# Performance work log

Measured on AMD Instinct MI355X. Metric: run time of the kernel, lower is better.

Reference implementation:

```python
import jax, jax.numpy as jnp
import numpy as np

N = 100000          # nodes
E = 600000          # directed edges in real graph
D = 128             # feature dim
LAYER_NUM = 16
ALPHA = 0.15        # args.alpha
DECLINE = 0.9       # args.decline
DECLINE_NEG = 0.5   # args.decline_neg


def setup_inputs() -> dict:
    key = jax.random.key(0)
    k1, k2, k3 = jax.random.split(key, 3)
    feat = jax.random.normal(k1, (N, D), dtype=jnp.float32)
    edge_index = jax.random.randint(k2, (2, E), 0, N, dtype=jnp.int64)
    # 60 sampled negative edges per layer; mirrored in reference -> 120 = round_even(20*E/N)
    neg_edge_index = jax.random.randint(k3, (LAYER_NUM, 2, 60), 0, N, dtype=jnp.int64)
    return {"feat": feat, "edge_index": edge_index, "neg_edge_index": neg_edge_index}


def _spmm(row, col, vals, x, n):
    # y[i] = sum_{e: row[e]==i} vals[e] * x[col[e]]
    return jax.ops.segment_sum(vals[:, None] * x[col], row, num_segments=n)


def reference(feat, edge_index, neg_edge_index):
    n = feat.shape[0]
    row, col = edge_index[0], edge_index[1]
    # symmetric_normalize_adjacency: D^{-1/2} A D^{-1/2} (row-sum degree)
    deg = jax.ops.segment_sum(jnp.ones_like(row, dtype=feat.dtype), row, num_segments=n)
    dis = jnp.where(deg > 0, deg ** -0.5, 0.0)  # guard isolated nodes
    vals = dis[row] * dis[col]

    edge_num = 2 * neg_edge_index.shape[2]  # mirrored -> even, matches (k+1)//2*2
    c = edge_num / n + 2.0                   # re-normalization of (2I - A_neg)

    beta = 1.0
    beta_neg = 1.0
    x = feat
    acc = jnp.zeros_like(feat)
    for l in range(LAYER_NUM):
        # negative adjacency: random edges, symmetrized
        nr = jnp.concatenate([neg_edge_index[l, 0], neg_edge_index[l, 1]])
        nc = jnp.concatenate([neg_edge_index[l, 1], neg_edge_index[l, 0]])
        neg_sp = jax.ops.segment_sum(x[nc], nr, num_segments=n)  # A_neg @ x
        # neg_A_hat = (2I - A_neg)/c ; inv_lazy_A = (1-bn) I + bn neg_A_hat
        inv_x = (1.0 - beta_neg) * x + beta_neg * (2.0 * x - neg_sp) / c
        # lazy_A = (1-b) I + b A_hat
        x = (1.0 - beta) * x + beta * _spmm(row, col, vals, x, n)
        acc = acc + 0.5 * (x + inv_x)
        beta *= DECLINE
        beta_neg *= DECLINE_NEG
    return ALPHA * feat + (1.0 - ALPHA) * (acc / float(LAYER_NUM))
```

## Files before the change

kernel.cpp:

```cpp
#include <hip/hip_runtime.h>
#include <hip/hip_fp16.h>

#define NN 100000
#define NE 600000
#define DD 128
#define NL 16
#define SCAN_B 1024
#define SCAN_NB ((NN + SCAN_B - 1) / SCAN_B)


__global__ void k_deg(const int* __restrict__ ei, int* __restrict__ deg) {
    int e = blockIdx.x * blockDim.x + threadIdx.x;
    if (e < NE) atomicAdd(&deg[ei[e]], 1);
}

__global__ void k_dis(const int* __restrict__ deg, float* __restrict__ dis) {
    int i = blockIdx.x * blockDim.x + threadIdx.x;
    if (i >= NN) return;
    int d = deg[i];
    dis[i] = d > 0 ? rsqrtf((float)d) : 0.f;
}

__global__ void k_bsum(const int* __restrict__ cnt, int* __restrict__ bsum) {
    __shared__ int sh[SCAN_B];
    int i = blockIdx.x * SCAN_B + threadIdx.x;
    sh[threadIdx.x] = (i < NN) ? cnt[i] : 0;
    __syncthreads();
    for (int off = SCAN_B / 2; off > 0; off >>= 1) {
        if (threadIdx.x < off) sh[threadIdx.x] += sh[threadIdx.x + off];
        __syncthreads();
    }
    if (threadIdx.x == 0) bsum[blockIdx.x] = sh[0];
}

__global__ void k_bscan(int* __restrict__ bsum) {
    if (threadIdx.x == 0) {
        int run = 0;
        for (int i = 0; i < SCAN_NB; ++i) { int v = bsum[i]; bsum[i] = run; run += v; }
    }
}

__global__ void k_scan2(const int* __restrict__ cnt, const int* __restrict__ bsum,
                        int* __restrict__ rowptr) {
    __shared__ int sh[SCAN_B];
    int i = blockIdx.x * SCAN_B + threadIdx.x;
    sh[threadIdx.x] = (i < NN) ? cnt[i] : 0;
    __syncthreads();
    for (int off = 1; off < SCAN_B; off <<= 1) {
        int t = (threadIdx.x >= off) ? sh[threadIdx.x - off] : 0;
        __syncthreads();
        sh[threadIdx.x] += t;
        __syncthreads();
    }
    if (i < NN) rowptr[i + 1] = bsum[blockIdx.x] + sh[threadIdx.x];
    if (blockIdx.x == 0 && threadIdx.x == 0) rowptr[0] = 0;
}

__global__ void k_fill(const int* __restrict__ ei, const float* __restrict__ dis,
                       const int* __restrict__ rowptr, int* __restrict__ cursor,
                       int2* __restrict__ edges) {
    int e = blockIdx.x * blockDim.x + threadIdx.x;
    if (e >= NE) return;
    int r = ei[e], c = ei[NE + e];
    float v = dis[r] * dis[c];
    int pos = rowptr[r] + atomicAdd(&cursor[r], 1);
    edges[pos] = make_int2(c, __float_as_int(v));
}

__global__ void k_cvt(const float* __restrict__ f, __half* __restrict__ h) {
    int i = blockIdx.x * blockDim.x + threadIdx.x;
    const float4 v = reinterpret_cast<const float4*>(f)[i];
    __half2 a = __floats2half2_rn(v.x, v.y);
    __half2 b = __floats2half2_rn(v.z, v.w);
    uint2 o;
    o.x = *reinterpret_cast<uint*>(&a);
    o.y = *reinterpret_cast<uint*>(&b);
    reinterpret_cast<uint2*>(h)[i] = o;
}

__device__ __forceinline__ void acc8(float* s, uint4 g, float v) {
    const __half2* h = reinterpret_cast<const __half2*>(&g);
    float2 f0 = __half22float2(h[0]);
    float2 f1 = __half22float2(h[1]);
    float2 f2 = __half22float2(h[2]);
    float2 f3 = __half22float2(h[3]);
    s[0] += v * f0.x; s[1] += v * f0.y; s[2] += v * f1.x; s[3] += v * f1.y;
    s[4] += v * f2.x; s[5] += v * f2.y; s[6] += v * f3.x; s[7] += v * f3.y;
}

template<int MODE>
__global__ __launch_bounds__(256) void k_layer(const int* __restrict__ rowptr,
                                               const int2* __restrict__ edges,
                                               const __half* __restrict__ xo,
                                               __half* __restrict__ xn,
                                               float* __restrict__ acc,
                                               const float* __restrict__ feat,
                                               float fb, float c0, float c1) {
    const int qw = threadIdx.x >> 4;
    const int lane = threadIdx.x & 15;
    const int r = blockIdx.x * 16 + qw;
    if (r >= NN) return;
    int p = rowptr[r];
    const int end = rowptr[r + 1];
    const int d8 = lane * 8;
    float s[8] = {0.f, 0.f, 0.f, 0.f, 0.f, 0.f, 0.f, 0.f};
    for (; p + 3 < end; p += 4) {
        int2 e0 = edges[p];
        int2 e1 = edges[p + 1];
        int2 e2 = edges[p + 2];
        int2 e3 = edges[p + 3];
        const uint4 g0 = *reinterpret_cast<const uint4*>(xo + (size_t)e0.x * DD + d8);
        const uint4 g1 = *reinterpret_cast<const uint4*>(xo + (size_t)e1.x * DD + d8);
        const uint4 g2 = *reinterpret_cast<const uint4*>(xo + (size_t)e2.x * DD + d8);
        const uint4 g3 = *reinterpret_cast<const uint4*>(xo + (size_t)e3.x * DD + d8);
        acc8(s, g0, __int_as_float(e0.y));
        acc8(s, g1, __int_as_float(e1.y));
        acc8(s, g2, __int_as_float(e2.y));
        acc8(s, g3, __int_as_float(e3.y));
    }
    for (; p < end; ++p) {
        int2 ev = edges[p];
        const uint4 gv = *reinterpret_cast<const uint4*>(xo + (size_t)ev.x * DD + d8);
        acc8(s, gv, __int_as_float(ev.y));
    }
    const size_t ih = (size_t)r * DD + d8;
    const uint4 ou = *reinterpret_cast<const uint4*>(xo + ih);
    float o[8];
    {
        const __half2* h = reinterpret_cast<const __half2*>(&ou);
        float2 f0 = __half22float2(h[0]);
        float2 f1 = __half22float2(h[1]);
        float2 f2 = __half22float2(h[2]);
        float2 f3 = __half22float2(h[3]);
        o[0] = f0.x; o[1] = f0.y; o[2] = f1.x; o[3] = f1.y;
        o[4] = f2.x; o[5] = f2.y; o[6] = f3.x; o[7] = f3.y;
    }
    float n[8];
#pragma unroll
    for (int k = 0; k < 8; ++k) n[k] = (1.f - fb) * o[k] + fb * s[k];

    if (MODE == 3) {
        const float4 fA = *reinterpret_cast<const float4*>(feat + ih);
        const float4 fB = *reinterpret_cast<const float4*>(feat + ih + 4);
        const float4 aA = *reinterpret_cast<const float4*>(acc + ih);
        const float4 aB = *reinterpret_cast<const float4*>(acc + ih + 4);
        float4 oA, oB;
        oA.x = 0.15f * fA.x + c0 * (aA.x + 0.5f * n[0]);
        oA.y = 0.15f * fA.y + c0 * (aA.y + 0.5f * n[1]);
        oA.z = 0.15f * fA.z + c0 * (aA.z + 0.5f * n[2]);
        oA.w = 0.15f * fA.w + c0 * (aA.w + 0.5f * n[3]);
        oB.x = 0.15f * fB.x + c0 * (aB.x + 0.5f * n[4]);
        oB.y = 0.15f * fB.y + c0 * (aB.y + 0.5f * n[5]);
        oB.z = 0.15f * fB.z + c0 * (aB.z + 0.5f * n[6]);
        oB.w = 0.15f * fB.w + c0 * (aB.w + 0.5f * n[7]);
        *reinterpret_cast<float4*>(acc + ih) = oA;
        *reinterpret_cast<float4*>(acc + ih + 4) = oB;
    } else {
        __half2 p0 = __floats2half2_rn(n[0], n[1]);
        __half2 p1 = __floats2half2_rn(n[2], n[3]);
        __half2 p2 = __floats2half2_rn(n[4], n[5]);
        __half2 p3 = __floats2half2_rn(n[6], n[7]);
        uint4 w;
        w.x = *reinterpret_cast<uint*>(&p0);
        w.y = *reinterpret_cast<uint*>(&p1);
        w.z = *reinterpret_cast<uint*>(&p2);
        w.w = *reinterpret_cast<uint*>(&p3);
        *reinterpret_cast<uint4*>(xn + ih) = w;
        if (MODE == 1) {
            float4 aA, aB;
            aA.x = c0 * o[0] + c1 * n[0];
            aA.y = c0 * o[1] + c1 * n[1];
            aA.z = c0 * o[2] + c1 * n[2];
            aA.w = c0 * o[3] + c1 * n[3];
            aB.x = c0 * o[4] + c1 * n[4];
            aB.y = c0 * o[5] + c1 * n[5];
            aB.z = c0 * o[6] + c1 * n[6];
            aB.w = c0 * o[7] + c1 * n[7];
            *reinterpret_cast<float4*>(acc + ih) = aA;
            *reinterpret_cast<float4*>(acc + ih + 4) = aB;
        } else if (MODE == 2) {
            float4 aA = *reinterpret_cast<const float4*>(acc + ih);
            float4 aB = *reinterpret_cast<const float4*>(acc + ih + 4);
            aA.x += c0 * o[0] + c1 * n[0];
            aA.y += c0 * o[1] + c1 * n[1];
            aA.z += c0 * o[2] + c1 * n[2];
            aA.w += c0 * o[3] + c1 * n[3];
            aB.x += c0 * o[4] + c1 * n[4];
            aB.y += c0 * o[5] + c1 * n[5];
            aB.z += c0 * o[6] + c1 * n[6];
            aB.w += c0 * o[7] + c1 * n[7];
            *reinterpret_cast<float4*>(acc + ih) = aA;
            *reinterpret_cast<float4*>(acc + ih + 4) = aB;
        }
    }
}

__global__ void k_neg(const int* __restrict__ nl, const __half* __restrict__ x,
                      float* __restrict__ acc, float coef) {
    int tid = blockIdx.x * blockDim.x + threadIdx.x;
    int e = tid >> 5;
    if (e >= 120) return;
    int d4 = (tid & 31) << 2;
    int r = nl[e];
    int c = (e < 60) ? nl[60 + e] : nl[e - 60];
    const uint2 g = *reinterpret_cast<const uint2*>(x + (size_t)c * DD + d4);
    const __half2* h = reinterpret_cast<const __half2*>(&g);
    float2 f0 = __half22float2(h[0]);
    float2 f1 = __half22float2(h[1]);
    float* ap = acc + (size_t)r * DD + d4;
    atomicAdd(ap + 0, coef * f0.x);
    atomicAdd(ap + 1, coef * f0.y);
    atomicAdd(ap + 2, coef * f1.x);
    atomicAdd(ap + 3, coef * f1.y);
}

extern "C" void kernel_launch(void* const* d_in, const int* in_sizes, int n_in,
                              void* d_out, int out_size, void* d_ws, size_t ws_size,
                              hipStream_t stream) {
    const float* feat = (const float*)d_in[0];
    const int* ei = (const int*)d_in[1];
    const int* negei = (const int*)d_in[2];
    float* out = (float*)d_out;

    __half* xh0 = (__half*)d_ws;
    __half* xha = xh0 + (size_t)NN * DD;
    __half* xhb = xha + (size_t)NN * DD;
    int2* edges = (int2*)(xhb + (size_t)NN * DD);
    int* rowptr = (int*)(edges + NE);
    int* deg = rowptr + (NN + 1);
    float* dis = (float*)(deg + NN);
    int* bsum = (int*)(dis + NN);

    hipMemsetAsync(deg, 0, NN * sizeof(int), stream);
    k_deg<<<(NE + 255) / 256, 256, 0, stream>>>(ei, deg);
    k_dis<<<(NN + 255) / 256, 256, 0, stream>>>(deg, dis);
    k_bsum<<<SCAN_NB, SCAN_B, 0, stream>>>(deg, bsum);
    k_bscan<<<1, 64, 0, stream>>>(bsum);
    k_scan2<<<SCAN_NB, SCAN_B, 0, stream>>>(deg, bsum, rowptr);
    hipMemsetAsync(deg, 0, NN * sizeof(int), stream);
    k_fill<<<(NE + 255) / 256, 256, 0, stream>>>(ei, dis, rowptr, deg, edges);
    k_cvt<<<(NN * DD / 4) / 256, 256, 0, stream>>>(feat, xh0);

    const double cc = 120.0 / 100000.0 + 2.0;
    double bv[NL], coef[NL + 1], negco[NL];
    {
        double b = 1.0, bn = 1.0;
        for (int l = 0; l < NL; ++l) {
            double al = (1.0 - bn) + 2.0 * bn / cc;
            bv[l] = b;
            coef[l] = 0.5 * al + (l > 0 ? 0.5 : 0.0);
            negco[l] = -0.5 * bn / cc;
            b *= 0.9;
            bn *= 0.5;
        }
    }

    const int lg = (NN + 15) / 16;

    for (int l = 0; l < NL - 1; ++l) {
        const __half* xo = (l == 0) ? xh0 : ((l & 1) ? xha : xhb);
        __half* xn = (l & 1) ? xhb : xha;
        float fb = (float)bv[l];
        if (l == 0) {
            k_layer<1><<<lg, 256, 0, stream>>>(rowptr, edges, xo, xn, out, feat,
                                               fb, (float)coef[0], (float)coef[1]);
        } else if ((l & 1) == 0) {
            k_layer<2><<<lg, 256, 0, stream>>>(rowptr, edges, xo, xn, out, feat,
                                               fb, (float)coef[l], (float)coef[l + 1]);
        } else {
            k_layer<0><<<lg, 256, 0, stream>>>(rowptr, edges, xo, xn, out, feat,
                                               fb, 0.f, 0.f);
        }
        k_neg<<<(120 * 32 + 255) / 256, 256, 0, stream>>>(negei + l * 120, xo, out,
                                                          (float)negco[l]);
    }
    {
        const __half* xo = xha;
        k_neg<<<(120 * 32 + 255) / 256, 256, 0, stream>>>(negei + 15 * 120, xo, out,
                                                          (float)negco[15]);
        k_layer<3><<<lg, 256, 0, stream>>>(rowptr, edges, xo, nullptr, out, feat,
                                           (float)bv[15], 0.85f / 16.f, 0.f);
    }
}
```

Baseline: 725.9 us.

## Split feature dimension into 32-wide chunks so each layer's working set fits cache

Runs the whole 16-layer propagation separately for each of four 32-column feature slices. Each slice uses compact half-precision ping-pong buffers and a float accumulator, which should shrink the gathered working set enough to stay L2/MALL resident. Within a row, four groups of lanes now split the edge list and combine partial sums with shuffles. The cost is four times as many kernel launches, and each slice re-reads the CSR edges and row pointers.

```diff
diff --git a/kernel.cpp b/kernel.cpp
--- a/kernel.cpp
+++ b/kernel.cpp
@@ -5,6 +5,8 @@
 #define NE 600000
 #define DD 128
 #define NL 16
+#define CW 32
+#define NCH (DD / CW)
 #define SCAN_B 1024
 #define SCAN_NB ((NN + SCAN_B - 1) / SCAN_B)
 
@@ -67,15 +69,23 @@
     edges[pos] = make_int2(c, __float_as_int(v));
 }
 
-__global__ void k_cvt(const float* __restrict__ f, __half* __restrict__ h) {
-    int i = blockIdx.x * blockDim.x + threadIdx.x;
-    const float4 v = reinterpret_cast<const float4*>(f)[i];
-    __half2 a = __floats2half2_rn(v.x, v.y);
-    __half2 b = __floats2half2_rn(v.z, v.w);
-    uint2 o;
-    o.x = *reinterpret_cast<uint*>(&a);
-    o.y = *reinterpret_cast<uint*>(&b);
-    reinterpret_cast<uint2*>(h)[i] = o;
+__global__ void k_cvt_slice(const float* __restrict__ feat, __half* __restrict__ xc,
+                            int chunk) {
+    int t = blockIdx.x * blockDim.x + threadIdx.x;
+    if (t >= NN * 4) return;
+    int row = t >> 2, q = t & 3;
+    const float4 a = *reinterpret_cast<const float4*>(feat + (size_t)row * DD + chunk * CW + q * 8);
+    const float4 b = *reinterpret_cast<const float4*>(feat + (size_t)row * DD + chunk * CW + q * 8 + 4);
+    __half2 h0 = __floats2half2_rn(a.x, a.y);
+    __half2 h1 = __floats2half2_rn(a.z, a.w);
+    __half2 h2 = __floats2half2_rn(b.x, b.y);
+    __half2 h3 = __floats2half2_rn(b.z, b.w);
+    uint4 w;
+    w.x = *reinterpret_cast<uint*>(&h0);
+    w.y = *reinterpret_cast<uint*>(&h1);
+    w.z = *reinterpret_cast<uint*>(&h2);
+    w.w = *reinterpret_cast<uint*>(&h3);
+    *reinterpret_cast<uint4*>(xc + (size_t)row * CW + q * 8) = w;
 }
 
 __device__ __forceinline__ void acc8(float* s, uint4 g, float v) {
@@ -95,35 +105,38 @@
                                                __half* __restrict__ xn,
                                                float* __restrict__ acc,
                                                const float* __restrict__ feat,
-                                               float fb, float c0, float c1) {
-    const int qw = threadIdx.x >> 4;
-    const int lane = threadIdx.x & 15;
-    const int r = blockIdx.x * 16 + qw;
-    if (r >= NN) return;
-    int p = rowptr[r];
+                                               float* __restrict__ out,
+                                               float fb, float c0, float c1,
+                                               int chunk) {
+    const int tid = threadIdx.x;
+    const int r = blockIdx.x * 16 + (tid >> 4);
+    const int g = (tid >> 2) & 3;
+    const int q = tid & 3;
+    const int beg = rowptr[r];
     const int end = rowptr[r + 1];
-    const int d8 = lane * 8;
     float s[8] = {0.f, 0.f, 0.f, 0.f, 0.f, 0.f, 0.f, 0.f};
-    for (; p + 3 < end; p += 4) {
+    int p = beg + g;
+    for (; p + 4 < end; p += 8) {
         int2 e0 = edges[p];
-        int2 e1 = edges[p + 1];
-        int2 e2 = edges[p + 2];
-        int2 e3 = edges[p + 3];
-        const uint4 g0 = *reinterpret_cast<const uint4*>(xo + (size_t)e0.x * DD + d8);
-        const uint4 g1 = *reinterpret_cast<const uint4*>(xo + (size_t)e1.x * DD + d8);
-        const uint4 g2 = *reinterpret_cast<const uint4*>(xo + (size_t)e2.x * DD + d8);
-        const uint4 g3 = *reinterpret_cast<const uint4*>(xo + (size_t)e3.x * DD + d8);
+        int2 e1 = edges[p + 4];
+        const uint4 g0 = *reinterpret_cast<const uint4*>(xo + (size_t)e0.x * CW + q * 8);
+        const uint4 g1 = *reinterpret_cast<const uint4*>(xo + (size_t)e1.x * CW + q * 8);
         acc8(s, g0, __int_as_float(e0.y));
         acc8(s, g1, __int_as_float(e1.y));
-        acc8(s, g2, __int_as_float(e2.y));
-        acc8(s, g3, __int_as_float(e3.y));
-    }
-    for (; p < end; ++p) {
+    }
+    if (p < end) {
         int2 ev = edges[p];
-        const uint4 gv = *reinterpret_cast<const uint4*>(xo + (size_t)ev.x * DD + d8);
+        const uint4 gv = *reinterpret_cast<const uint4*>(xo + (size_t)ev.x * CW + q * 8);
         acc8(s, gv, __int_as_float(ev.y));
     }
-    const size_t ih = (size_t)r * DD + d8;
+#pragma unroll
+    for (int k = 0; k < 8; ++k) {
+        s[k] += __shfl_xor(s[k], 4);
+        s[k] += __shfl_xor(s[k], 8);
+    }
+    if (g != 0) return;
+
+    const size_t ih = (size_t)r * CW + q * 8;
     const uint4 ou = *reinterpret_cast<const uint4*>(xo + ih);
     float o[8];
     {
@@ -140,8 +153,9 @@
     for (int k = 0; k < 8; ++k) n[k] = (1.f - fb) * o[k] + fb * s[k];
 
     if (MODE == 3) {
-        const float4 fA = *reinterpret_cast<const float4*>(feat + ih);
-        const float4 fB = *reinterpret_cast<const float4*>(feat + ih + 4);
+        const size_t fi = (size_t)r * DD + chunk * CW + q * 8;
+        const float4 fA = *reinterpret_cast<const float4*>(feat + fi);
+        const float4 fB = *reinterpret_cast<const float4*>(feat + fi + 4);
         const float4 aA = *reinterpret_cast<const float4*>(acc + ih);
         const float4 aB = *reinterpret_cast<const float4*>(acc + ih + 4);
         float4 oA, oB;
@@ -153,8 +167,8 @@
         oB.y = 0.15f * fB.y + c0 * (aB.y + 0.5f * n[5]);
         oB.z = 0.15f * fB.z + c0 * (aB.z + 0.5f * n[6]);
         oB.w = 0.15f * fB.w + c0 * (aB.w + 0.5f * n[7]);
-        *reinterpret_cast<float4*>(acc + ih) = oA;
-        *reinterpret_cast<float4*>(acc + ih + 4) = oB;
+        *reinterpret_cast<float4*>(out + fi) = oA;
+        *reinterpret_cast<float4*>(out + fi + 4) = oB;
     } else {
         __half2 p0 = __floats2half2_rn(n[0], n[1]);
         __half2 p1 = __floats2half2_rn(n[2], n[3]);
@@ -198,16 +212,16 @@
 __global__ void k_neg(const int* __restrict__ nl, const __half* __restrict__ x,
                       float* __restrict__ acc, float coef) {
     int tid = blockIdx.x * blockDim.x + threadIdx.x;
-    int e = tid >> 5;
-    if (e >= 120) return;
-    int d4 = (tid & 31) << 2;
+    if (tid >= 120 * 8) return;
+    int e = tid >> 3;
+    int t8 = tid & 7;
     int r = nl[e];
     int c = (e < 60) ? nl[60 + e] : nl[e - 60];
-    const uint2 g = *reinterpret_cast<const uint2*>(x + (size_t)c * DD + d4);
+    const uint2 g = *reinterpret_cast<const uint2*>(x + (size_t)c * CW + t8 * 4);
     const __half2* h = reinterpret_cast<const __half2*>(&g);
     float2 f0 = __half22float2(h[0]);
     float2 f1 = __half22float2(h[1]);
-    float* ap = acc + (size_t)r * DD + d4;
+    float* ap = acc + (size_t)r * CW + t8 * 4;
     atomicAdd(ap + 0, coef * f0.x);
     atomicAdd(ap + 1, coef * f0.y);
     atomicAdd(ap + 2, coef * f1.x);
@@ -222,10 +236,11 @@
     const int* negei = (const int*)d_in[2];
     float* out = (float*)d_out;
 
-    __half* xh0 = (__half*)d_ws;
-    __half* xha = xh0 + (size_t)NN * DD;
-    __half* xhb = xha + (size_t)NN * DD;
-    int2* edges = (int2*)(xhb + (size_t)NN * DD);
+    __half* xc0 = (__half*)d_ws;
+    __half* xca = xc0 + (size_t)NN * CW;
+    __half* xcb = xca + (size_t)NN * CW;
+    float* accc = (float*)(xcb + (size_t)NN * CW);
+    int2* edges = (int2*)(accc + (size_t)NN * CW);
     int* rowptr = (int*)(edges + NE);
     int* deg = rowptr + (NN + 1);
     float* dis = (float*)(deg + NN);
@@ -239,7 +254,6 @@
     k_scan2<<<SCAN_NB, SCAN_B, 0, stream>>>(deg, bsum, rowptr);
     hipMemsetAsync(deg, 0, NN * sizeof(int), stream);
     k_fill<<<(NE + 255) / 256, 256, 0, stream>>>(ei, dis, rowptr, deg, edges);
-    k_cvt<<<(NN * DD / 4) / 256, 256, 0, stream>>>(feat, xh0);
 
     const double cc = 120.0 / 100000.0 + 2.0;
     double bv[NL], coef[NL + 1], negco[NL];
@@ -255,30 +269,33 @@
         }
     }
 
-    const int lg = (NN + 15) / 16;
-
-    for (int l = 0; l < NL - 1; ++l) {
-        const __half* xo = (l == 0) ? xh0 : ((l & 1) ? xha : xhb);
-        __half* xn = (l & 1) ? xhb : xha;
-        float fb = (float)bv[l];
-        if (l == 0) {
-            k_layer<1><<<lg, 256, 0, stream>>>(rowptr, edges, xo, xn, out, feat,
-                                               fb, (float)coef[0], (float)coef[1]);
-        } else if ((l & 1) == 0) {
-            k_layer<2><<<lg, 256, 0, stream>>>(rowptr, edges, xo, xn, out, feat,
-                                               fb, (float)coef[l], (float)coef[l + 1]);
-        } else {
-            k_layer<0><<<lg, 256, 0, stream>>>(rowptr, edges, xo, xn, out, feat,
-                                               fb, 0.f, 0.f);
+    const int lg = NN / 16;
+    const int cg = (NN * 4 + 255) / 256;
+    const int ng = (120 * 8 + 255) / 256;
+
+    for (int ch = 0; ch < NCH; ++ch) {
+        k_cvt_slice<<<cg, 256, 0, stream>>>(feat, xc0, ch);
+        for (int l = 0; l < NL - 1; ++l) {
+            const __half* xo = (l == 0) ? xc0 : ((l & 1) ? xca : xcb);
+            __half* xn = (l & 1) ? xcb : xca;
+            float fb = (float)bv[l];
+            if (l == 0) {
+                k_layer<1><<<lg, 256, 0, stream>>>(rowptr, edges, xo, xn, accc, feat, out,
+                                                   fb, (float)coef[0], (float)coef[1], ch);
+            } else if ((l & 1) == 0) {
+                k_layer<2><<<lg, 256, 0, stream>>>(rowptr, edges, xo, xn, accc, feat, out,
+                                                   fb, (float)coef[l], (float)coef[l + 1], ch);
+            } else {
+                k_layer<0><<<lg, 256, 0, stream>>>(rowptr, edges, xo, xn, accc, feat, out,
+                                                   fb, 0.f, 0.f, ch);
+            }
+            k_neg<<<ng, 256, 0, stream>>>(negei + l * 120, xo, accc, (float)negco[l]);
         }
-        k_neg<<<(120 * 32 + 255) / 256, 256, 0, stream>>>(negei + l * 120, xo, out,
-                                                          (float)negco[l]);
-    }
-    {
-        const __half* xo = xha;
-        k_neg<<<(120 * 32 + 255) / 256, 256, 0, stream>>>(negei + 15 * 120, xo, out,
-                                                          (float)negco[15]);
-        k_layer<3><<<lg, 256, 0, stream>>>(rowptr, edges, xo, nullptr, out, feat,
-                                           (float)bv[15], 0.85f / 16.f, 0.f);
-    }
-}
+        {
+            const __half* xo = xca;
+            k_neg<<<ng, 256, 0, stream>>>(negei + 15 * 120, xo, accc, (float)negco[15]);
+            k_layer<3><<<lg, 256, 0, stream>>>(rowptr, edges, xo, nullptr, accc, feat, out,
+                                               (float)bv[15], 0.85f / 16.f, 0.f, ch);
+        }
+    }
+}
```

New measurement: 1.247 ms. +71.8%, slower.

## Batch accumulator updates every four layers using a four-buffer feature ring

Applied to the files above, without the earlier changes.

Keeps four fp16 feature buffers in a ring so the fp32 accumulator is read and written once every four layers instead of every other layer. Each accumulating layer reads the two earlier snapshots and folds their contributions in. The 60-edge negative-sample scatter kernels are merged into one launch per four layers, and the separate dis kernel and the second memset are removed by computing rsqrt inside the fill kernel. The cost is extra fp16 reads of xm2 and xm1 in the accumulating layers, one more N×D fp16 buffer of workspace, and dropping the row bounds check, which relies on N being divisible by 16.

```diff
diff --git a/kernel.cpp b/kernel.cpp
--- a/kernel.cpp
+++ b/kernel.cpp
@@ -12,13 +12,6 @@
 __global__ void k_deg(const int* __restrict__ ei, int* __restrict__ deg) {
     int e = blockIdx.x * blockDim.x + threadIdx.x;
     if (e < NE) atomicAdd(&deg[ei[e]], 1);
-}
-
-__global__ void k_dis(const int* __restrict__ deg, float* __restrict__ dis) {
-    int i = blockIdx.x * blockDim.x + threadIdx.x;
-    if (i >= NN) return;
-    int d = deg[i];
-    dis[i] = d > 0 ? rsqrtf((float)d) : 0.f;
 }
 
 __global__ void k_bsum(const int* __restrict__ cnt, int* __restrict__ bsum) {
@@ -56,13 +49,14 @@
     if (blockIdx.x == 0 && threadIdx.x == 0) rowptr[0] = 0;
 }
 
-__global__ void k_fill(const int* __restrict__ ei, const float* __restrict__ dis,
+__global__ void k_fill(const int* __restrict__ ei, const int* __restrict__ deg,
                        const int* __restrict__ rowptr, int* __restrict__ cursor,
                        int2* __restrict__ edges) {
     int e = blockIdx.x * blockDim.x + threadIdx.x;
     if (e >= NE) return;
     int r = ei[e], c = ei[NE + e];
-    float v = dis[r] * dis[c];
+    int dr = deg[r], dc = deg[c];
+    float v = (dr > 0 ? rsqrtf((float)dr) : 0.f) * (dc > 0 ? rsqrtf((float)dc) : 0.f);
     int pos = rowptr[r] + atomicAdd(&cursor[r], 1);
     edges[pos] = make_int2(c, __float_as_int(v));
 }
@@ -88,18 +82,30 @@
     s[4] += v * f2.x; s[5] += v * f2.y; s[6] += v * f3.x; s[7] += v * f3.y;
 }
 
+__device__ __forceinline__ void cvt8(float* o, uint4 g) {
+    const __half2* h = reinterpret_cast<const __half2*>(&g);
+    float2 f0 = __half22float2(h[0]);
+    float2 f1 = __half22float2(h[1]);
+    float2 f2 = __half22float2(h[2]);
+    float2 f3 = __half22float2(h[3]);
+    o[0] = f0.x; o[1] = f0.y; o[2] = f1.x; o[3] = f1.y;
+    o[4] = f2.x; o[5] = f2.y; o[6] = f3.x; o[7] = f3.y;
+}
+
 template<int MODE>
 __global__ __launch_bounds__(256) void k_layer(const int* __restrict__ rowptr,
                                                const int2* __restrict__ edges,
                                                const __half* __restrict__ xo,
                                                __half* __restrict__ xn,
+                                               const __half* __restrict__ xm2,
+                                               const __half* __restrict__ xm1,
                                                float* __restrict__ acc,
                                                const float* __restrict__ feat,
-                                               float fb, float c0, float c1) {
+                                               float fb, float cA, float cB,
+                                               float c0, float c1) {
     const int qw = threadIdx.x >> 4;
     const int lane = threadIdx.x & 15;
     const int r = blockIdx.x * 16 + qw;
-    if (r >= NN) return;
     int p = rowptr[r];
     const int end = rowptr[r + 1];
     const int d8 = lane * 8;
@@ -124,17 +130,8 @@
         acc8(s, gv, __int_as_float(ev.y));
     }
     const size_t ih = (size_t)r * DD + d8;
-    const uint4 ou = *reinterpret_cast<const uint4*>(xo + ih);
     float o[8];
-    {
-        const __half2* h = reinterpret_cast<const __half2*>(&ou);
-        float2 f0 = __half22float2(h[0]);
-        float2 f1 = __half22float2(h[1]);
-        float2 f2 = __half22float2(h[2]);
-        float2 f3 = __half22float2(h[3]);
-        o[0] = f0.x; o[1] = f0.y; o[2] = f1.x; o[3] = f1.y;
-        o[4] = f2.x; o[5] = f2.y; o[6] = f3.x; o[7] = f3.y;
-    }
+    cvt8(o, *reinterpret_cast<const uint4*>(xo + ih));
     float n[8];
 #pragma unroll
     for (int k = 0; k < 8; ++k) n[k] = (1.f - fb) * o[k] + fb * s[k];
@@ -166,40 +163,44 @@
         w.z = *reinterpret_cast<uint*>(&p2);
         w.w = *reinterpret_cast<uint*>(&p3);
         *reinterpret_cast<uint4*>(xn + ih) = w;
-        if (MODE == 1) {
-            float4 aA, aB;
-            aA.x = c0 * o[0] + c1 * n[0];
-            aA.y = c0 * o[1] + c1 * n[1];
-            aA.z = c0 * o[2] + c1 * n[2];
-            aA.w = c0 * o[3] + c1 * n[3];
-            aB.x = c0 * o[4] + c1 * n[4];
-            aB.y = c0 * o[5] + c1 * n[5];
-            aB.z = c0 * o[6] + c1 * n[6];
-            aB.w = c0 * o[7] + c1 * n[7];
-            *reinterpret_cast<float4*>(acc + ih) = aA;
-            *reinterpret_cast<float4*>(acc + ih + 4) = aB;
-        } else if (MODE == 2) {
-            float4 aA = *reinterpret_cast<const float4*>(acc + ih);
-            float4 aB = *reinterpret_cast<const float4*>(acc + ih + 4);
-            aA.x += c0 * o[0] + c1 * n[0];
-            aA.y += c0 * o[1] + c1 * n[1];
-            aA.z += c0 * o[2] + c1 * n[2];
-            aA.w += c0 * o[3] + c1 * n[3];
-            aB.x += c0 * o[4] + c1 * n[4];
-            aB.y += c0 * o[5] + c1 * n[5];
-            aB.z += c0 * o[6] + c1 * n[6];
-            aB.w += c0 * o[7] + c1 * n[7];
-            *reinterpret_cast<float4*>(acc + ih) = aA;
-            *reinterpret_cast<float4*>(acc + ih + 4) = aB;
-        }
-    }
-}
-
-__global__ void k_neg(const int* __restrict__ nl, const __half* __restrict__ x,
-                      float* __restrict__ acc, float coef) {
+        if (MODE == 1 || MODE == 2) {
+            float m2[8], m1[8];
+            cvt8(m2, *reinterpret_cast<const uint4*>(xm2 + ih));
+            cvt8(m1, *reinterpret_cast<const uint4*>(xm1 + ih));
+            float t[8];
+#pragma unroll
+            for (int k = 0; k < 8; ++k)
+                t[k] = cA * m2[k] + cB * m1[k] + c0 * o[k] + c1 * n[k];
+            if (MODE == 1) {
+                float4 aA, aB;
+                aA.x = t[0]; aA.y = t[1]; aA.z = t[2]; aA.w = t[3];
+                aB.x = t[4]; aB.y = t[5]; aB.z = t[6]; aB.w = t[7];
+                *reinterpret_cast<float4*>(acc + ih) = aA;
+                *reinterpret_cast<float4*>(acc + ih + 4) = aB;
+            } else {
+                float4 aA = *reinterpret_cast<const float4*>(acc + ih);
+                float4 aB = *reinterpret_cast<const float4*>(acc + ih + 4);
+                aA.x += t[0]; aA.y += t[1]; aA.z += t[2]; aA.w += t[3];
+                aB.x += t[4]; aB.y += t[5]; aB.z += t[6]; aB.w += t[7];
+                *reinterpret_cast<float4*>(acc + ih) = aA;
+                *reinterpret_cast<float4*>(acc + ih + 4) = aB;
+            }
+        }
+    }
+}
+
+__global__ void k_neg4(const int* __restrict__ ng, const __half* __restrict__ s0,
+                       const __half* __restrict__ s1, const __half* __restrict__ s2,
+                       const __half* __restrict__ s3, float* __restrict__ acc,
+                       float n0, float n1, float n2, float n3) {
     int tid = blockIdx.x * blockDim.x + threadIdx.x;
-    int e = tid >> 5;
-    if (e >= 120) return;
+    int e4 = tid >> 5;
+    if (e4 >= 480) return;
+    int lg = e4 / 120;
+    int e = e4 - lg * 120;
+    const int* nl = ng + lg * 120;
+    const __half* x = (lg == 0) ? s0 : (lg == 1) ? s1 : (lg == 2) ? s2 : s3;
+    float coef = (lg == 0) ? n0 : (lg == 1) ? n1 : (lg == 2) ? n2 : n3;
     int d4 = (tid & 31) << 2;
     int r = nl[e];
     int c = (e < 60) ? nl[60 + e] : nl[e - 60];
@@ -222,27 +223,28 @@
     const int* negei = (const int*)d_in[2];
     float* out = (float*)d_out;
 
-    __half* xh0 = (__half*)d_ws;
-    __half* xha = xh0 + (size_t)NN * DD;
-    __half* xhb = xha + (size_t)NN * DD;
-    int2* edges = (int2*)(xhb + (size_t)NN * DD);
+    __half* S[4];
+    S[0] = (__half*)d_ws;
+    S[1] = S[0] + (size_t)NN * DD;
+    S[2] = S[1] + (size_t)NN * DD;
+    S[3] = S[2] + (size_t)NN * DD;
+    int2* edges = (int2*)(S[3] + (size_t)NN * DD);
     int* rowptr = (int*)(edges + NE);
     int* deg = rowptr + (NN + 1);
-    float* dis = (float*)(deg + NN);
-    int* bsum = (int*)(dis + NN);
+    int* cursor = deg + NN;
+    int* bsum = cursor + NN;
 
     hipMemsetAsync(deg, 0, NN * sizeof(int), stream);
+    hipMemsetAsync(cursor, 0, NN * sizeof(int), stream);
     k_deg<<<(NE + 255) / 256, 256, 0, stream>>>(ei, deg);
-    k_dis<<<(NN + 255) / 256, 256, 0, stream>>>(deg, dis);
     k_bsum<<<SCAN_NB, SCAN_B, 0, stream>>>(deg, bsum);
     k_bscan<<<1, 64, 0, stream>>>(bsum);
     k_scan2<<<SCAN_NB, SCAN_B, 0, stream>>>(deg, bsum, rowptr);
-    hipMemsetAsync(deg, 0, NN * sizeof(int), stream);
-    k_fill<<<(NE + 255) / 256, 256, 0, stream>>>(ei, dis, rowptr, deg, edges);
-    k_cvt<<<(NN * DD / 4) / 256, 256, 0, stream>>>(feat, xh0);
+    k_fill<<<(NE + 255) / 256, 256, 0, stream>>>(ei, deg, rowptr, cursor, edges);
+    k_cvt<<<(NN * DD / 4) / 256, 256, 0, stream>>>(feat, S[0]);
 
     const double cc = 120.0 / 100000.0 + 2.0;
-    double bv[NL], coef[NL + 1], negco[NL];
+    double bv[NL], coef[NL], negco[NL];
     {
         double b = 1.0, bn = 1.0;
         for (int l = 0; l < NL; ++l) {
@@ -255,30 +257,38 @@
         }
     }
 
-    const int lg = (NN + 15) / 16;
+    const int lg = NN / 16;
+    const int ngrid = (480 * 32 + 255) / 256;
 
     for (int l = 0; l < NL - 1; ++l) {
-        const __half* xo = (l == 0) ? xh0 : ((l & 1) ? xha : xhb);
-        __half* xn = (l & 1) ? xhb : xha;
+        const __half* xo = S[l & 3];
+        __half* xn = S[(l + 1) & 3];
         float fb = (float)bv[l];
-        if (l == 0) {
-            k_layer<1><<<lg, 256, 0, stream>>>(rowptr, edges, xo, xn, out, feat,
-                                               fb, (float)coef[0], (float)coef[1]);
-        } else if ((l & 1) == 0) {
-            k_layer<2><<<lg, 256, 0, stream>>>(rowptr, edges, xo, xn, out, feat,
-                                               fb, (float)coef[l], (float)coef[l + 1]);
+        bool accl = (l == 2 || l == 6 || l == 10 || l == 14);
+        if (l == 2) {
+            k_layer<1><<<lg, 256, 0, stream>>>(rowptr, edges, xo, xn,
+                                               S[0], S[1], out, feat, fb,
+                                               (float)coef[0], (float)coef[1],
+                                               (float)coef[2], (float)coef[3]);
+        } else if (accl) {
+            k_layer<2><<<lg, 256, 0, stream>>>(rowptr, edges, xo, xn,
+                                               S[(l - 2) & 3], S[(l - 1) & 3], out, feat, fb,
+                                               (float)coef[l - 2], (float)coef[l - 1],
+                                               (float)coef[l], (float)coef[l + 1]);
         } else {
-            k_layer<0><<<lg, 256, 0, stream>>>(rowptr, edges, xo, xn, out, feat,
-                                               fb, 0.f, 0.f);
-        }
-        k_neg<<<(120 * 32 + 255) / 256, 256, 0, stream>>>(negei + l * 120, xo, out,
-                                                          (float)negco[l]);
-    }
-    {
-        const __half* xo = xha;
-        k_neg<<<(120 * 32 + 255) / 256, 256, 0, stream>>>(negei + 15 * 120, xo, out,
-                                                          (float)negco[15]);
-        k_layer<3><<<lg, 256, 0, stream>>>(rowptr, edges, xo, nullptr, out, feat,
-                                           (float)bv[15], 0.85f / 16.f, 0.f);
-    }
-}
+            k_layer<0><<<lg, 256, 0, stream>>>(rowptr, edges, xo, xn,
+                                               nullptr, nullptr, nullptr, nullptr, fb,
+                                               0.f, 0.f, 0.f, 0.f);
+        }
+        if (accl) {
+            int g = (l - 2) / 4;
+            k_neg4<<<ngrid, 256, 0, stream>>>(negei + 4 * g * 120,
+                                              S[0], S[1], S[2], S[3], out,
+                                              (float)negco[4 * g], (float)negco[4 * g + 1],
+                                              (float)negco[4 * g + 2], (float)negco[4 * g + 3]);
+        }
+    }
+    k_layer<3><<<lg, 256, 0, stream>>>(rowptr, edges, S[3], nullptr,
+                                       nullptr, nullptr, out, feat,
+                                       (float)bv[15], 0.f, 0.f, 0.85f / 16.f, 0.f);
+}
```

New measurement: 670.6 us. -7.6%, faster.
